# Kernel optimization log

Measured on AMD Instinct MI355X. Metric: run time of the kernel, lower is better.

## Reference

```python
import jax, jax.numpy as jnp
import numpy as np

DIM, HEADS = 1536, 12
HD = DIM // HEADS            # 128 head dim
C = HD // 2                  # 64 complex (pair) dim
C0 = C - 2 * (C // 3)        # 22 (temporal axis)
C1 = C // 3                  # 21 (each spatial axis)
MAX_POS = 1024
F_, H_, W_ = 9, 22, 22
SEQ = F_ * H_ * W_           # 4356
NCLASS = 2
EPS = 1e-6


def _rope_tables():
    # Wan rope_params: theta = 10000, per-axis half-dims C0, C1, C1.
    def ang(half):
        inv = 1.0 / (10000.0 ** (np.arange(0, 2 * half, 2) / (2 * half)))
        return np.outer(np.arange(MAX_POS), inv)
    a = np.concatenate([ang(C0), ang(C1), ang(C1)], axis=1)  # [MAX_POS, C]
    return jnp.asarray(np.cos(a), jnp.float32), jnp.asarray(np.sin(a), jnp.float32)


def setup_inputs() -> dict:
    key = jax.random.key(0)
    ks = jax.random.split(key, 6)
    s = 1.0 / np.sqrt(DIM)
    def lin(k):
        k1, k2 = jax.random.split(k)
        return (jax.random.uniform(k1, (DIM, DIM), jnp.float32, -s, s),
                jax.random.uniform(k2, (DIM,), jnp.float32, -s, s))
    Wq, bq = lin(ks[0]); Wk, bk = lin(ks[1]); Wv, bv = lin(ks[2]); Wo, bo = lin(ks[3])
    fc, fs = _rope_tables()
    masks = (jax.random.uniform(ks[4], (NCLASS, H_ * W_)) < 0.5).astype(jnp.float32)
    x = jax.random.normal(ks[5], (1, SEQ, DIM), jnp.float32)
    return {"x": x, "Wq": Wq, "bq": bq, "Wk": Wk, "bk": bk, "Wv": Wv, "bv": bv,
            "Wo": Wo, "bo": bo, "gq": jnp.ones((DIM,), jnp.float32),
            "gk": jnp.ones((DIM,), jnp.float32), "freqs_cos": fc, "freqs_sin": fs,
            "ref_target_masks": masks, "f": F_, "h": H_, "w": W_}


def _rmsnorm(x, g):
    return x * jax.lax.rsqrt(jnp.mean(x * x, axis=-1, keepdims=True) + EPS) * g


def _grid_cs(tab, f, h, w):
    # per-position (f,h,w) rope table -> [f*h*w, C]
    p0 = jnp.broadcast_to(tab[:f, None, None, :C0], (f, h, w, C0))
    p1 = jnp.broadcast_to(tab[None, :h, None, C0:C0 + C1], (f, h, w, C1))
    p2 = jnp.broadcast_to(tab[None, None, :w, C0 + C1:], (f, h, w, C1))
    return jnp.concatenate([p0, p1, p2], axis=-1).reshape(f * h * w, C)


def _rope(x, cos, sin):
    # x: [b,s,n,d]; pairs are interleaved along d (view_as_complex semantics)
    b, s, n, d = x.shape
    xr = x.reshape(b, s, n, d // 2, 2)
    a, bi = xr[..., 0], xr[..., 1]
    cos = cos[None, :, None, :]
    sin = sin[None, :, None, :]
    out = jnp.stack([a * cos - bi * sin, a * sin + bi * cos], axis=-1)
    return out.reshape(b, s, n, d)


def reference(x, Wq, bq, Wk, bk, Wv, bv, Wo, bo, gq, gk, freqs_cos, freqs_sin,
              ref_target_masks, f, h, w):
    b, s, _ = x.shape
    n, d = HEADS, HD
    q = _rmsnorm(x @ Wq.T + bq, gq).reshape(b, s, n, d)
    k = _rmsnorm(x @ Wk.T + bk, gk).reshape(b, s, n, d)
    v = (x @ Wv.T + bv).reshape(b, s, n, d)
    cos = _grid_cs(freqs_cos, f, h, w)
    sin = _grid_cs(freqs_sin, f, h, w)
    q = _rope(q, cos, sin)
    k = _rope(k, cos, sin)
    scale = 1.0 / np.sqrt(d).astype(np.float32)
    # full (window_size == (-1,-1)) attention; seq_lens == s so k_lens mask is identity
    scores = jnp.einsum('bsnd,btnd->bnst', q, k) * scale
    p = jax.nn.softmax(scores, axis=-1)
    o = jnp.einsum('bnst,btnd->bsnd', p, v).reshape(b, s, n * d)
    out = o @ Wo.T + bo
    # aux attention map vs reference-frame keys (first h*w spatial tokens), no-grad path
    xs = h * w
    ref_k = k[:, :xs]
    s2 = jnp.einsum('bsnd,btnd->bnst', q * scale, ref_k)
    p2 = jax.nn.softmax(s2, axis=-1)                       # [b,n,s,xs]
    m = ref_target_masks                                   # [c,xs]
    maps = jnp.einsum('bnst,ct->cbns', p2, m) / jnp.sum(m, axis=-1)[:, None, None, None]
    attn_map = maps.mean(axis=2).reshape(-1, s)            # mean over heads -> [c*b, s]
    return out, attn_map
```

## Files before the change

kernel.cpp:

```cpp
#include <hip/hip_runtime.h>
#include <hip/hip_bf16.h>
#include <math.h>

constexpr int SEQ   = 4356;
constexpr int DIM   = 1536;
constexpr int HEADS = 12;
constexpr int HD    = 128;
constexpr int CH    = 64;
constexpr int C0c   = 22;
constexpr int C1c   = 21;
constexpr int WWc   = 22;
constexpr int HHWW  = 484;
constexpr int XS    = 484;
constexpr int KVB   = 32;
constexpr int NT    = (SEQ + KVB - 1) / KVB;
constexpr int SEQP  = 4416;
constexpr size_t SD = (size_t)SEQ * DIM;

typedef float f32x4 __attribute__((ext_vector_type(4)));
typedef short bf16x8 __attribute__((ext_vector_type(8)));
typedef short bf16x4 __attribute__((ext_vector_type(4)));

__device__ inline unsigned short f2bf(float f) {
  union { float f; unsigned u; } x; x.f = f;
  return (unsigned short)((x.u + 0x7FFFu + ((x.u >> 16) & 1u)) >> 16);
}

#define GLD16(g, l)                                                                        \
  __builtin_amdgcn_global_load_lds((const __attribute__((address_space(1))) unsigned*)    \
                                       (const void*)(g),                                  \
                                   (__attribute__((address_space(3))) unsigned*)(void*)(l),\
                                   16, 0, 0)

__global__ __launch_bounds__(256) void prep_kernel(const float* __restrict__ mask,
                                                   float* __restrict__ amap,
                                                   float* __restrict__ cnt,
                                                   float4* __restrict__ msk4) {
  int t = threadIdx.x;
  for (int i = t; i < 2 * SEQ; i += 256) amap[i] = 0.f;
  for (int i = t; i < 512; i += 256) {
    float4 v;
    v.x = (i < XS) ? mask[i] : 0.f;
    v.y = (i < XS) ? mask[XS + i] : 0.f;
    v.z = (i < XS) ? 1.f : 0.f;
    v.w = 0.f;
    msk4[i] = v;
  }
  float c0 = 0.f, c1 = 0.f;
  for (int i = t; i < XS; i += 256) { c0 += mask[i]; c1 += mask[XS + i]; }
  __shared__ float red0[256];
  __shared__ float red1[256];
  red0[t] = c0; red1[t] = c1;
  __syncthreads();
  for (int off = 128; off > 0; off >>= 1) {
    if (t < off) { red0[t] += red0[t + off]; red1[t] += red1[t + off]; }
    __syncthreads();
  }
  if (t == 0) { cnt[0] = red0[0]; cnt[1] = red1[0]; }
}

__global__ __launch_bounds__(256) void padzero(unsigned short* __restrict__ vt) {
  const int pad = SEQP - SEQ;
  const int total = DIM * pad;
  for (int i = blockIdx.x * 256 + threadIdx.x; i < total; i += gridDim.x * 256) {
    const int d = i / pad, c = i - d * pad;
    vt[(size_t)d * SEQP + SEQ + c] = 0;
  }
}

__global__ __launch_bounds__(256) void to_bf16(const float* __restrict__ in,
                                               unsigned short* __restrict__ out, int n4) {
  for (int i = blockIdx.x * 256 + threadIdx.x; i < n4; i += gridDim.x * 256) {
    const float4 v = ((const float4*)in)[i];
    ushort4 o;
    o.x = f2bf(v.x); o.y = f2bf(v.y); o.z = f2bf(v.z); o.w = f2bf(v.w);
    ((ushort4*)out)[i] = o;
  }
}

__global__ __launch_bounds__(256) void to_bf16_w(const float* __restrict__ W0, const float* __restrict__ W1,
                                                 const float* __restrict__ W2, const float* __restrict__ W3,
                                                 unsigned short* __restrict__ o0, unsigned short* __restrict__ o1,
                                                 unsigned short* __restrict__ o2, unsigned short* __restrict__ o3,
                                                 int n4) {
  const int z = blockIdx.z;
  const float* in = (z == 0) ? W0 : (z == 1) ? W1 : (z == 2) ? W2 : W3;
  unsigned short* out = (z == 0) ? o0 : (z == 1) ? o1 : (z == 2) ? o2 : o3;
  for (int i = blockIdx.x * 256 + threadIdx.x; i < n4; i += gridDim.x * 256) {
    const float4 v = ((const float4*)in)[i];
    ushort4 o;
    o.x = f2bf(v.x); o.y = f2bf(v.y); o.z = f2bf(v.z); o.w = f2bf(v.w);
    ((ushort4*)out)[i] = o;
  }
}

__global__ __launch_bounds__(256) void gemm_qkv(const unsigned short* __restrict__ A,
                                                const unsigned short* __restrict__ B0,
                                                const unsigned short* __restrict__ B1,
                                                const unsigned short* __restrict__ B2,
                                                const float* __restrict__ bq,
                                                const float* __restrict__ bk,
                                                const float* __restrict__ bv,
                                                float* __restrict__ o0,
                                                float* __restrict__ o1,
                                                unsigned short* __restrict__ vtout,
                                                int M) {
  __shared__ unsigned short As[128 * 64];
  __shared__ unsigned short Bs[128 * 64];
  const int z = blockIdx.z;
  const unsigned short* B = (z == 0) ? B0 : (z == 1) ? B1 : B2;
  const float* bias = (z == 0) ? bq : (z == 1) ? bk : bv;
  const int t    = threadIdx.x;
  const int lane = t & 63;
  const int w    = t >> 6;
  const int wr   = w >> 1, wc = w & 1;
  const int bm = blockIdx.x * 128, bn = blockIdx.y * 128;
  const int lq = lane & 15, lg = lane >> 4;
  f32x4 acc[4][4] = {};
  for (int k0 = 0; k0 < DIM; k0 += 64) {
#pragma unroll
    for (int i = 0; i < 4; ++i) {
      const int idx = i * 256 + t;
      const int row = idx >> 3;
      const int c8  = (idx & 7) * 8;
      const int ga  = min(bm + row, M - 1);
      GLD16(A + (size_t)ga * DIM + k0 + c8, As + idx * 8);
      const int gb  = bn + row;
      GLD16(B + (size_t)gb * DIM + k0 + c8, Bs + idx * 8);
    }
    __syncthreads();
#pragma unroll
    for (int kk = 0; kk < 2; ++kk) {
      bf16x8 af[4], bf[4];
#pragma unroll
      for (int m = 0; m < 4; ++m)
        af[m] = *(const bf16x8*)(As + (wr * 64 + m * 16 + lq) * 64 + kk * 32 + lg * 8);
#pragma unroll
      for (int n = 0; n < 4; ++n)
        bf[n] = *(const bf16x8*)(Bs + (wc * 64 + n * 16 + lq) * 64 + kk * 32 + lg * 8);
#pragma unroll
      for (int m = 0; m < 4; ++m)
#pragma unroll
        for (int n = 0; n < 4; ++n)
          acc[m][n] = __builtin_amdgcn_mfma_f32_16x16x32_bf16(af[m], bf[n], acc[m][n], 0, 0, 0);
    }
    __syncthreads();
  }
#pragma unroll
  for (int n = 0; n < 4; ++n) {
    const int col = bn + wc * 64 + n * 16 + lq;
    const float bv2 = bias[col];
#pragma unroll
    for (int m = 0; m < 4; ++m) {
      const int rm = bm + wr * 64 + m * 16 + lg * 4;
      if (z < 2) {
        float* C = (z == 0) ? o0 : o1;
#pragma unroll
        for (int r = 0; r < 4; ++r) {
          const int row = rm + r;
          if (row < M) C[(size_t)row * DIM + col] = acc[m][n][r] + bv2;
        }
      } else {
        if (rm < M) {
          bf16x4 o;
#pragma unroll
          for (int r = 0; r < 4; ++r) o[r] = (short)f2bf(acc[m][n][r] + bv2);
          *(bf16x4*)(vtout + (size_t)col * SEQP + rm) = o;
        }
      }
    }
  }
}

__global__ __launch_bounds__(256) void gemm_mfma(const unsigned short* __restrict__ A,
                                                 const unsigned short* __restrict__ B,
                                                 const float* __restrict__ bias,
                                                 float* __restrict__ C, int M) {
  __shared__ unsigned short As[128 * 64];
  __shared__ unsigned short Bs[128 * 64];
  const int t    = threadIdx.x;
  const int lane = t & 63;
  const int w    = t >> 6;
  const int wr   = w >> 1, wc = w & 1;
  const int bm = blockIdx.x * 128, bn = blockIdx.y * 128;
  const int lq = lane & 15, lg = lane >> 4;
  f32x4 acc[4][4] = {};
  for (int k0 = 0; k0 < DIM; k0 += 64) {
#pragma unroll
    for (int i = 0; i < 4; ++i) {
      const int idx = i * 256 + t;
      const int row = idx >> 3;
      const int c8  = (idx & 7) * 8;
      const int ga  = min(bm + row, M - 1);
      GLD16(A + (size_t)ga * DIM + k0 + c8, As + idx * 8);
      const int gb  = bn + row;
      GLD16(B + (size_t)gb * DIM + k0 + c8, Bs + idx * 8);
    }
    __syncthreads();
#pragma unroll
    for (int kk = 0; kk < 2; ++kk) {
      bf16x8 af[4], bf[4];
#pragma unroll
      for (int m = 0; m < 4; ++m)
        af[m] = *(const bf16x8*)(As + (wr * 64 + m * 16 + lq) * 64 + kk * 32 + lg * 8);
#pragma unroll
      for (int n = 0; n < 4; ++n)
        bf[n] = *(const bf16x8*)(Bs + (wc * 64 + n * 16 + lq) * 64 + kk * 32 + lg * 8);
#pragma unroll
      for (int m = 0; m < 4; ++m)
#pragma unroll
        for (int n = 0; n < 4; ++n)
          acc[m][n] = __builtin_amdgcn_mfma_f32_16x16x32_bf16(af[m], bf[n], acc[m][n], 0, 0, 0);
    }
    __syncthreads();
  }
#pragma unroll
  for (int n = 0; n < 4; ++n) {
    const int col = bn + wc * 64 + n * 16 + lq;
    const float bv = bias[col];
#pragma unroll
    for (int m = 0; m < 4; ++m) {
      const int rm = bm + wr * 64 + m * 16 + lg * 4;
#pragma unroll
      for (int r = 0; r < 4; ++r) {
        const int row = rm + r;
        if (row < M) C[(size_t)row * DIM + col] = acc[m][n][r] + bv;
      }
    }
  }
}

__global__ __launch_bounds__(256) void rms_rope2(const float* __restrict__ qy,
                                                 const float* __restrict__ ky,
                                                 const float* __restrict__ gq,
                                                 const float* __restrict__ gk,
                                                 const float* __restrict__ fcos,
                                                 const float* __restrict__ fsin,
                                                 unsigned short* __restrict__ qout,
                                                 unsigned short* __restrict__ kout) {
  const int z = blockIdx.y;
  const float* y = z ? ky : qy;
  const float* g = z ? gk : gq;
  unsigned short* outb = z ? kout : qout;
  const float scale = z ? 1.0f : 0.08838834764831845f;
  const int s = blockIdx.x;
  const float* row = y + (size_t)s * DIM;
  const int t = threadIdx.x;
  float ss = 0.f;
  for (int i = t; i < DIM / 4; i += 256) {
    const float4 v = ((const float4*)row)[i];
    ss += v.x * v.x + v.y * v.y + v.z * v.z + v.w * v.w;
  }
#pragma unroll
  for (int off = 1; off < 64; off <<= 1) ss += __shfl_xor(ss, off);
  __shared__ float wred[4];
  if ((t & 63) == 0) wred[t >> 6] = ss;
  __syncthreads();
  const float tot = wred[0] + wred[1] + wred[2] + wred[3];
  const float rs = rsqrtf(tot * (1.0f / DIM) + 1e-6f);
  const int fi  = s / HHWW;
  const int rem = s - fi * HHWW;
  const int hi  = rem / WWc;
  const int wi  = rem - hi * WWc;
  for (int p = t; p < DIM / 2; p += 256) {
    const int head = p >> 6;
    const int c    = p & 63;
    const int idx  = head * HD + 2 * c;
    const int trow = (c < C0c) ? fi : ((c < C0c + C1c) ? hi : wi);
    const float co = fcos[trow * CH + c];
    const float si = fsin[trow * CH + c];
    const float a  = row[idx] * rs * g[idx];
    const float b  = row[idx + 1] * rs * g[idx + 1];
    ushort2 pr;
    pr.x = f2bf((a * co - b * si) * scale);
    pr.y = f2bf((a * si + b * co) * scale);
    *(ushort2*)(outb + (size_t)s * DIM + idx) = pr;
  }
}

#define SOFT_QS(QS, SACC, MAP_, LAST_, KBV)                                                \
  {                                                                                        \
    float sv[8];                                                                           \
    _Pragma("unroll")                                                                      \
    for (int i = 0; i < 8; ++i) {                                                          \
      float v = SACC[i >> 2][i & 3];                                                       \
      if (LAST_) { const int key = (KBV) + (i >> 2) * 16 + lg * 4 + (i & 3);               \
                   if (key >= SEQ) v = -1e30f; }                                           \
      sv[i] = __expf(v);                                                                   \
      ls[QS] += sv[i];                                                                     \
    }                                                                                      \
    if (MAP_) {                                                                            \
      _Pragma("unroll")                                                                    \
      for (int i = 0; i < 8; ++i) {                                                        \
        const int key = (KBV) + (i >> 2) * 16 + lg * 4 + (i & 3);                          \
        const float4 mv = Msk[key];                                                       \
        n0[QS] = fmaf(sv[i], mv.x, n0[QS]);                                                \
        n1[QS] = fmaf(sv[i], mv.y, n1[QS]);                                                \
        d2[QS] = fmaf(sv[i], mv.z, d2[QS]);                                                \
      }                                                                                    \
    }                                                                                      \
    _Pragma("unroll")                                                                      \
    for (int kbi = 0; kbi < 2; ++kbi) {                                                    \
      unsigned r0, r1;                                                                     \
      asm("v_cvt_pk_bf16_f32 %0, %1, %2" : "=v"(r0) : "v"(sv[kbi*4+0]), "v"(sv[kbi*4+1])); \
      asm("v_cvt_pk_bf16_f32 %0, %1, %2" : "=v"(r1) : "v"(sv[kbi*4+2]), "v"(sv[kbi*4+3])); \
      uint2 pw; pw.x = r0; pw.y = r1;                                                      \
      *(uint2*)&Pw[QS][lq][kbi * 16 + lg * 4] = pw;                                        \
    }                                                                                      \
  }

#define TILE_BODY(KB_, MAP_, LAST_, PRE_)                                                  \
  {                                                                                        \
    const int kb_ = (KB_);                                                                 \
    const int cur_ = (kb_ >> 5) & 1;                                                       \
    const unsigned short* Kc = Ks[cur_];                                                   \
    const unsigned short* Vc = Vs[cur_];                                                   \
    if (PRE_) {                                                                            \
      unsigned short* Kn = Ks[cur_ ^ 1];                                                   \
      unsigned short* Vn = Vs[cur_ ^ 1];                                                   \
      const int kbn = kb_ + KVB;                                                           \
      _Pragma("unroll")                                                                    \
      for (int j = 0; j < 2; ++j) {                                                        \
        const int ck = t + j * 256;                                                        \
        const int kr = ck >> 4, ksl = ck & 15;                                             \
        GLD16(kh + (size_t)min(kbn + kr, SEQ - 1) * DIM + ((ksl ^ (kr & 7)) * 8),          \
              Kn + ck * 8);                                                                \
        const int vd = ck >> 2, vsl = ck & 3;                                              \
        GLD16(vh + (size_t)vd * SEQP + kbn + ((vsl ^ ((vd >> 1) & 3)) * 8),                \
              Vn + ck * 8);                                                                \
      }                                                                                    \
    }                                                                                      \
    f32x4 sacc0[2] = {}, sacc1[2] = {};                                                    \
    __builtin_amdgcn_s_setprio(1);                                                         \
    _Pragma("unroll")                                                                      \
    for (int kbi = 0; kbi < 2; ++kbi) {                                                    \
      const int krow = kbi * 16 + lq;                                                      \
      _Pragma("unroll")                                                                    \
      for (int c = 0; c < 4; ++c) {                                                        \
        const bf16x8 kf = *(const bf16x8*)(Kc + (krow * 16 + ((c * 4 + lg) ^ (krow & 7))) * 8); \
        sacc0[kbi] = __builtin_amdgcn_mfma_f32_16x16x32_bf16(kf, qf0[c], sacc0[kbi], 0, 0, 0);  \
        sacc1[kbi] = __builtin_amdgcn_mfma_f32_16x16x32_bf16(kf, qf1[c], sacc1[kbi], 0, 0, 0);  \
      }                                                                                    \
    }                                                                                      \
    __builtin_amdgcn_s_setprio(0);                                                         \
    SOFT_QS(0, sacc0, MAP_, LAST_, kb_)                                                    \
    SOFT_QS(1, sacc1, MAP_, LAST_, kb_)                                                    \
    {                                                                                      \
      const bf16x8 pf0 = *(const bf16x8*)&Pw[0][lq][lg * 8];                               \
      const bf16x8 pf1 = *(const bf16x8*)&Pw[1][lq][lg * 8];                               \
      __builtin_amdgcn_s_setprio(1);                                                       \
      _Pragma("unroll")                                                                    \
      for (int db = 0; db < 8; ++db) {                                                     \
        const int vd = db * 16 + lq;                                                       \
        const bf16x8 vf = *(const bf16x8*)(Vc + (vd * 4 + (lg ^ ((vd >> 1) & 3))) * 8);    \
        acc0[db] = __builtin_amdgcn_mfma_f32_16x16x32_bf16(vf, pf0, acc0[db], 0, 0, 0);    \
        acc1[db] = __builtin_amdgcn_mfma_f32_16x16x32_bf16(vf, pf1, acc1[db], 0, 0, 0);    \
      }                                                                                    \
      __builtin_amdgcn_s_setprio(0);                                                       \
    }                                                                                      \
    if (PRE_) __syncthreads();                                                             \
  }

__global__ __launch_bounds__(256, 3) void flash_mfma(const unsigned short* __restrict__ qbuf,
                                                     const unsigned short* __restrict__ kbuf,
                                                     const unsigned short* __restrict__ vt,
                                                     const float4* __restrict__ msk4,
                                                     const float* __restrict__ cnt,
                                                     unsigned short* __restrict__ ob,
                                                     float* __restrict__ amap) {
  const int h    = blockIdx.y;
  const int t    = threadIdx.x;
  const int w    = t >> 6;
  const int lane = t & 63;
  const int lq   = lane & 15, lg = lane >> 4;
  const int qbase = blockIdx.x * 128 + w * 32;

  __shared__ __align__(16) unsigned short Ks[2][KVB * 128];
  __shared__ __align__(16) unsigned short Vs[2][128 * KVB];
  __shared__ __align__(16) unsigned short Plds[4][2][16][40];
  __shared__ float4 Msk[512];
  unsigned short (*Pw)[16][40] = Plds[w];

  const unsigned short* kh = kbuf + h * HD;
  const unsigned short* vh = vt + (size_t)(h * HD) * SEQP;

  for (int i = t; i < 512; i += 256) Msk[i] = msk4[i];

  const int qsrc0 = min(qbase + lq, SEQ - 1);
  const int qsrc1 = min(qbase + 16 + lq, SEQ - 1);
  bf16x8 qf0[4], qf1[4];
#pragma unroll
  for (int c = 0; c < 4; ++c) {
    qf0[c] = *(const bf16x8*)(qbuf + (size_t)qsrc0 * DIM + h * HD + c * 32 + lg * 8);
    qf1[c] = *(const bf16x8*)(qbuf + (size_t)qsrc1 * DIM + h * HD + c * 32 + lg * 8);
  }

  f32x4 acc0[8] = {}, acc1[8] = {};
  float ls[2] = {0.f, 0.f};
  float d2[2] = {0.f, 0.f}, n0[2] = {0.f, 0.f}, n1[2] = {0.f, 0.f};

#pragma unroll
  for (int j = 0; j < 2; ++j) {
    const int ck = t + j * 256;
    const int kr = ck >> 4, ksl = ck & 15;
    GLD16(kh + (size_t)min(kr, SEQ - 1) * DIM + ((ksl ^ (kr & 7)) * 8), Ks[0] + ck * 8);
    const int vd = ck >> 2, vsl = ck & 3;
    GLD16(vh + (size_t)vd * SEQP + ((vsl ^ ((vd >> 1) & 3)) * 8), Vs[0] + ck * 8);
  }
  __syncthreads();

  for (int tile = 0; tile < 16; ++tile)         TILE_BODY(tile * KVB, true,  false, true);
  for (int tile = 16; tile < NT - 1; ++tile)    TILE_BODY(tile * KVB, false, false, true);
  TILE_BODY((NT - 1) * KVB, false, true, false);

#pragma unroll
  for (int qs = 0; qs < 2; ++qs) {
    ls[qs] += __shfl_xor(ls[qs], 16);
    ls[qs] += __shfl_xor(ls[qs], 32);
  }
  {
    const int qrow = qbase + lq;
    if (qrow < SEQ) {
      const float inv = 1.f / ls[0];
#pragma unroll
      for (int db = 0; db < 8; ++db) {
        bf16x4 o;
#pragma unroll
        for (int r = 0; r < 4; ++r) o[r] = (short)f2bf(acc0[db][r] * inv);
        *(bf16x4*)(ob + (size_t)qrow * DIM + h * HD + db * 16 + lg * 4) = o;
      }
    }
  }
  {
    const int qrow = qbase + 16 + lq;
    if (qrow < SEQ) {
      const float inv = 1.f / ls[1];
#pragma unroll
      for (int db = 0; db < 8; ++db) {
        bf16x4 o;
#pragma unroll
        for (int r = 0; r < 4; ++r) o[r] = (short)f2bf(acc1[db][r] * inv);
        *(bf16x4*)(ob + (size_t)qrow * DIM + h * HD + db * 16 + lg * 4) = o;
      }
    }
  }
#pragma unroll
  for (int qs = 0; qs < 2; ++qs) {
    float dd = d2[qs], a0 = n0[qs], a1 = n1[qs];
    dd += __shfl_xor(dd, 16); dd += __shfl_xor(dd, 32);
    a0 += __shfl_xor(a0, 16); a0 += __shfl_xor(a0, 32);
    a1 += __shfl_xor(a1, 16); a1 += __shfl_xor(a1, 32);
    const int qrow = qbase + qs * 16 + lq;
    if (lane < 16 && qrow < SEQ) {
      const float invd = 1.f / (dd * (float)HEADS);
      atomicAdd(&amap[qrow],       a0 * invd / cnt[0]);
      atomicAdd(&amap[SEQ + qrow], a1 * invd / cnt[1]);
    }
  }
}

extern "C" void kernel_launch(void* const* d_in, const int* in_sizes, int n_in,
                              void* d_out, int out_size, void* d_ws, size_t ws_size,
                              hipStream_t stream) {
  const float* x    = (const float*)d_in[0];
  const float* Wq   = (const float*)d_in[1];
  const float* bq   = (const float*)d_in[2];
  const float* Wk   = (const float*)d_in[3];
  const float* bk   = (const float*)d_in[4];
  const float* Wv   = (const float*)d_in[5];
  const float* bv   = (const float*)d_in[6];
  const float* Wo   = (const float*)d_in[7];
  const float* bo   = (const float*)d_in[8];
  const float* gq   = (const float*)d_in[9];
  const float* gk   = (const float*)d_in[10];
  const float* fc   = (const float*)d_in[11];
  const float* fs   = (const float*)d_in[12];
  const float* mask = (const float*)d_in[13];

  float* out  = (float*)d_out;
  float* amap = out + SD;
  float* f32a = out;

  float* f32b        = (float*)d_ws;
  unsigned short* xb = (unsigned short*)(f32b + SD);
  unsigned short* qb = xb + SD;
  unsigned short* kb = qb + SD;
  unsigned short* vt = kb + SD;
  unsigned short* wqb = vt + (size_t)DIM * SEQP;
  unsigned short* wkb = wqb + (size_t)DIM * DIM;
  unsigned short* wvb = wkb + (size_t)DIM * DIM;
  unsigned short* wob = wvb + (size_t)DIM * DIM;
  float4* msk4 = (float4*)(wob + (size_t)DIM * DIM);
  float* cnt  = (float*)(msk4 + 512);
  unsigned short* ob = (unsigned short*)f32b;

  prep_kernel<<<1, 256, 0, stream>>>(mask, amap, cnt, msk4);
  padzero<<<64, 256, 0, stream>>>(vt);
  to_bf16<<<2048, 256, 0, stream>>>(x, xb, (int)(SD / 4));
  constexpr int W4 = DIM * DIM / 4;
  to_bf16_w<<<dim3(512, 1, 4), 256, 0, stream>>>(Wq, Wk, Wv, Wo, wqb, wkb, wvb, wob, W4);

  const dim3 gg((SEQ + 127) / 128, DIM / 128, 3);
  gemm_qkv<<<gg, 256, 0, stream>>>(xb, wqb, wkb, wvb, bq, bk, bv, f32a, f32b, vt, SEQ);

  rms_rope2<<<dim3(SEQ, 2), 256, 0, stream>>>(f32a, f32b, gq, gk, fc, fs, qb, kb);

  const dim3 fg((SEQ + 127) / 128, HEADS);
  flash_mfma<<<fg, 256, 0, stream>>>(qb, kb, vt, msk4, cnt, ob, amap);

  const dim3 go((SEQ + 127) / 128, DIM / 128);
  gemm_mfma<<<go, 256, 0, stream>>>(ob, wob, bo, out, SEQ);
}
```

Baseline: 402.9 us.

## Triple-buffer K/V tiles with prefetch distance two and vmcnt-based waits

Replaces the double-buffered K/V LDS pipeline with a three-stage ring. Each tile now prefetches two tiles ahead and waits with s_waitcnt vmcnt(4) plus a raw barrier instead of a trailing __syncthreads, so global loads get more time in flight. The mask table is read from global memory instead of an LDS copy, which frees LDS for the third buffer. Launch bounds drop from 3 to 2 blocks per SM; that raises the register budget but may cut occupancy. The hand-set vmcnt count also depends on the exact number of outstanding loads per thread.

```diff
diff --git a/kernel.cpp b/kernel.cpp
--- a/kernel.cpp
+++ b/kernel.cpp
@@ -293,7 +293,7 @@
       _Pragma("unroll")                                                                    \
       for (int i = 0; i < 8; ++i) {                                                        \
         const int key = (KBV) + (i >> 2) * 16 + lg * 4 + (i & 3);                          \
-        const float4 mv = Msk[key];                                                       \
+        const float4 mv = msk4[key];                                                       \
         n0[QS] = fmaf(sv[i], mv.x, n0[QS]);                                                \
         n1[QS] = fmaf(sv[i], mv.y, n1[QS]);                                                \
         d2[QS] = fmaf(sv[i], mv.z, d2[QS]);                                                \
@@ -309,16 +309,21 @@
     }                                                                                      \
   }
 
-#define TILE_BODY(KB_, MAP_, LAST_, PRE_)                                                  \
+#define TILE_BODY(KB_, MAP_, LAST_, PRE_, W0_)                                             \
   {                                                                                        \
     const int kb_ = (KB_);                                                                 \
-    const int cur_ = (kb_ >> 5) & 1;                                                       \
-    const unsigned short* Kc = Ks[cur_];                                                   \
-    const unsigned short* Vc = Vs[cur_];                                                   \
+    const int tt_ = kb_ >> 5;                                                              \
+    const unsigned short* Kc = Ks[tt_ % 3];                                                \
+    const unsigned short* Vc = Vs[tt_ % 3];                                                \
+    if (W0_) { asm volatile("s_waitcnt vmcnt(0)" ::: "memory"); }                          \
+    else     { asm volatile("s_waitcnt vmcnt(4)" ::: "memory"); }                          \
+    __builtin_amdgcn_s_barrier();                                                          \
+    __builtin_amdgcn_sched_barrier(0);                                                     \
     if (PRE_) {                                                                            \
-      unsigned short* Kn = Ks[cur_ ^ 1];                                                   \
-      unsigned short* Vn = Vs[cur_ ^ 1];                                                   \
-      const int kbn = kb_ + KVB;                                                           \
+      const int pb_ = (tt_ + 2) % 3;                                                       \
+      unsigned short* Kn = Ks[pb_];                                                        \
+      unsigned short* Vn = Vs[pb_];                                                        \
+      const int kbn = kb_ + 2 * KVB;                                                       \
       _Pragma("unroll")                                                                    \
       for (int j = 0; j < 2; ++j) {                                                        \
         const int ck = t + j * 256;                                                        \
@@ -358,10 +363,9 @@
       }                                                                                    \
       __builtin_amdgcn_s_setprio(0);                                                       \
     }                                                                                      \
-    if (PRE_) __syncthreads();                                                             \
-  }
-
-__global__ __launch_bounds__(256, 3) void flash_mfma(const unsigned short* __restrict__ qbuf,
+  }
+
+__global__ __launch_bounds__(256, 2) void flash_mfma(const unsigned short* __restrict__ qbuf,
                                                      const unsigned short* __restrict__ kbuf,
                                                      const unsigned short* __restrict__ vt,
                                                      const float4* __restrict__ msk4,
@@ -375,16 +379,13 @@
   const int lq   = lane & 15, lg = lane >> 4;
   const int qbase = blockIdx.x * 128 + w * 32;
 
-  __shared__ __align__(16) unsigned short Ks[2][KVB * 128];
-  __shared__ __align__(16) unsigned short Vs[2][128 * KVB];
+  __shared__ __align__(16) unsigned short Ks[3][KVB * 128];
+  __shared__ __align__(16) unsigned short Vs[3][128 * KVB];
   __shared__ __align__(16) unsigned short Plds[4][2][16][40];
-  __shared__ float4 Msk[512];
   unsigned short (*Pw)[16][40] = Plds[w];
 
   const unsigned short* kh = kbuf + h * HD;
   const unsigned short* vh = vt + (size_t)(h * HD) * SEQP;
-
-  for (int i = t; i < 512; i += 256) Msk[i] = msk4[i];
 
   const int qsrc0 = min(qbase + lq, SEQ - 1);
   const int qsrc1 = min(qbase + 16 + lq, SEQ - 1);
@@ -407,11 +408,19 @@
     const int vd = ck >> 2, vsl = ck & 3;
     GLD16(vh + (size_t)vd * SEQP + ((vsl ^ ((vd >> 1) & 3)) * 8), Vs[0] + ck * 8);
   }
-  __syncthreads();
-
-  for (int tile = 0; tile < 16; ++tile)         TILE_BODY(tile * KVB, true,  false, true);
-  for (int tile = 16; tile < NT - 1; ++tile)    TILE_BODY(tile * KVB, false, false, true);
-  TILE_BODY((NT - 1) * KVB, false, true, false);
+#pragma unroll
+  for (int j = 0; j < 2; ++j) {
+    const int ck = t + j * 256;
+    const int kr = ck >> 4, ksl = ck & 15;
+    GLD16(kh + (size_t)min(KVB + kr, SEQ - 1) * DIM + ((ksl ^ (kr & 7)) * 8), Ks[1] + ck * 8);
+    const int vd = ck >> 2, vsl = ck & 3;
+    GLD16(vh + (size_t)vd * SEQP + KVB + ((vsl ^ ((vd >> 1) & 3)) * 8), Vs[1] + ck * 8);
+  }
+
+  for (int tile = 0; tile < 16; ++tile)         TILE_BODY(tile * KVB, true,  false, true,  false);
+  for (int tile = 16; tile < NT - 2; ++tile)    TILE_BODY(tile * KVB, false, false, true,  false);
+  TILE_BODY((NT - 2) * KVB, false, false, false, false);
+  TILE_BODY((NT - 1) * KVB, false, true,  false, true);
 
 #pragma unroll
   for (int qs = 0; qs < 2; ++qs) {
```

New measurement: 400.1 us. About the same (-0.7%).
